# Performance work log

Measured on AMD Instinct MI355X. Metric: run time of the kernel, lower is better.

Reference implementation:

```python
import jax, jax.numpy as jnp
import numpy as np

N, E, B = 10000, 100000, 64
VOCAB, EMB, H = 5000, 100, 2000
LAYERS = 4


def setup_inputs() -> dict:
    key = jax.random.key(0)
    ks = jax.random.split(key, 12)
    s = 0.02
    tokens = jax.random.randint(ks[0], (N,), 0, VOCAB)
    edge_index = jax.random.randint(ks[1], (2, E), 0, N)
    batch = (jnp.arange(N) * B) // N  # sorted node->graph ids, every graph nonempty
    return {
        "tokens": tokens,
        "edge_index": edge_index,
        "batch": batch,
        "embed_table": jax.random.normal(ks[2], (VOCAB, EMB), jnp.float32) * s,
        "W_ggc": jax.random.normal(ks[3], (LAYERS, H, H), jnp.float32) * s,
        "W_ih": jax.random.normal(ks[4], (3 * H, H), jnp.float32) * s,
        "W_hh": jax.random.normal(ks[5], (3 * H, H), jnp.float32) * s,
        "b_ih": jnp.zeros((3 * H,), jnp.float32),
        "b_hh": jnp.zeros((3 * H,), jnp.float32),
        "conv1_w": jax.random.normal(ks[6], (50, 1, 3), jnp.float32) * s,
        "conv1_b": jnp.zeros((50,), jnp.float32),
        "conv2_w": jax.random.normal(ks[7], (100, 50, 3), jnp.float32) * s,
        "conv2_b": jnp.zeros((100,), jnp.float32),
        "conv3_w": jax.random.normal(ks[8], (150, 100, 3), jnp.float32) * s,
        "conv3_b": jnp.zeros((150,), jnp.float32),
        "lin1_w": jax.random.normal(ks[9], (500, 10950), jnp.float32) * s,
        "lin1_b": jnp.zeros((500,), jnp.float32),
        "lin2_w": jax.random.normal(ks[10], (4, 500), jnp.float32) * s,
        "lin2_b": jnp.zeros((4,), jnp.float32),
    }


def _conv1d(x, w, b):
    # x: [B, Cin, L], w: [Cout, Cin, K] -> [B, Cout, L-K+1] (VALID, like nn.Conv1d)
    y = jax.lax.conv_general_dilated(x, w, (1,), "VALID",
                                     dimension_numbers=("NCH", "OIH", "NCH"))
    return y + b[None, :, None]


def _maxpool3(x):
    # MaxPool1d(kernel=3, stride=3), floor mode (VALID)
    return jax.lax.reduce_window(x, -jnp.inf, jax.lax.max, (1, 1, 3), (1, 1, 3), "VALID")


def _gru_cell(m, h, W_ih, W_hh, b_ih, b_hh):
    gi = m @ W_ih.T + b_ih  # [N, 3H]
    gh = h @ W_hh.T + b_hh
    ir, iz, inn = jnp.split(gi, 3, axis=-1)
    hr, hz, hn = jnp.split(gh, 3, axis=-1)
    r = jax.nn.sigmoid(ir + hr)
    z = jax.nn.sigmoid(iz + hz)
    n = jnp.tanh(inn + r * hn)
    return (1.0 - z) * n + z * h


def reference(tokens, edge_index, batch, embed_table, W_ggc, W_ih, W_hh, b_ih, b_hh,
              conv1_w, conv1_b, conv2_w, conv2_b, conv3_w, conv3_b,
              lin1_w, lin1_b, lin2_w, lin2_b):
    src, dst = edge_index[0], edge_index[1]
    n_nodes = tokens.shape[0]
    # embedding + pad to GatedGraphConv width (PyG zero-pads when in < out)
    h = embed_table[tokens]                               # [N, 100]
    h = jnp.pad(h, ((0, 0), (0, H - h.shape[1])))         # [N, 2000]
    # GatedGraphConv: per-layer linear -> scatter-add over edges -> GRU update
    for i in range(LAYERS):
        m = h @ W_ggc[i]                                  # [N, H]
        agg = jax.ops.segment_sum(m[src], dst, num_segments=n_nodes)  # [N, H]
        h = _gru_cell(agg, h, W_ih, W_hh, b_ih, b_hh)
    x = jax.nn.relu(h)
    # global_max_pool over graphs
    pooled = jax.ops.segment_max(x, batch, num_segments=B)  # [B, 2000]
    x = pooled[:, None, :]                                  # [B, 1, 2000]
    x = _maxpool3(jax.nn.relu(_conv1d(x, conv1_w, conv1_b)))  # [B,50,666]
    x = _maxpool3(jax.nn.relu(_conv1d(x, conv2_w, conv2_b)))  # [B,100,221]
    x = _maxpool3(jax.nn.relu(_conv1d(x, conv3_w, conv3_b)))  # [B,150,73]
    x = x.reshape(x.shape[0], -1)                             # [B, 10950]
    x = jax.nn.relu(x @ lin1_w.T + lin1_b)
    # dropout is identity in eval mode
    x = jax.nn.relu(x @ lin2_w.T + lin2_b)
    return x
```

## Files before the change

### kernel.cpp

```cpp
#include <hip/hip_runtime.h>
#include <math.h>

#define N_NODES 10000
#define N_EDGES 100000
#define NB      64
#define EMB     100
#define H       2000
#define LAYERS  4

#define C1_OC 50
#define C1_L  666
#define C2_OC 100
#define C2_L  221
#define C3_OC 150
#define C3_L  73
#define LIN1_IN  10950
#define LIN1_OUT 500

#define SEG  2048
#define MP   10240
#define NW   2048
#define KK2  4096
#define NPACK 8192
#define NT   (KK2 / 64)

using half8 = __attribute__((ext_vector_type(8))) _Float16;
using f32x4 = __attribute__((ext_vector_type(4))) float;

__device__ inline void gload16(const void* g, void* l) {
  __builtin_amdgcn_global_load_lds(
      (const __attribute__((address_space(1))) unsigned int*)g,
      (__attribute__((address_space(3))) unsigned int*)l, 16, 0, 0);
}

__global__ void embed16_kernel(const int* __restrict__ tokens,
                               const float* __restrict__ table,
                               _Float16* __restrict__ h) {
  int n = blockIdx.x;
  int tok = tokens[n];
  for (int c = threadIdx.x; c < SEG; c += 256) {
    float v = (c < EMB) ? table[tok * EMB + c] : 0.f;
    h[(size_t)n * SEG + c] = (_Float16)v;
  }
}

__global__ void hist_kernel(const int* __restrict__ dst, int* __restrict__ counts, int e) {
  int i = blockIdx.x * 256 + threadIdx.x;
  if (i < e) atomicAdd(&counts[dst[i]], 1);
}

__global__ void scan_kernel(const int* __restrict__ counts, int* __restrict__ row_off, int n) {
  __shared__ int sums[1024];
  int tid = threadIdx.x;
  const int CH = (n + 1023) / 1024;
  int start = tid * CH;
  int local = 0;
  for (int i = 0; i < CH; i++)
    if (start + i < n) local += counts[start + i];
  sums[tid] = local;
  __syncthreads();
  for (int off = 1; off < 1024; off <<= 1) {
    int v = (tid >= off) ? sums[tid - off] : 0;
    __syncthreads();
    sums[tid] += v;
    __syncthreads();
  }
  int run = (tid > 0) ? sums[tid - 1] : 0;
  for (int i = 0; i < CH; i++)
    if (start + i < n) { row_off[start + i] = run; run += counts[start + i]; }
  if (tid == 1023) row_off[n] = run;
}

__global__ void scatter_kernel(const int* __restrict__ src, const int* __restrict__ dst,
                               const int* __restrict__ row_off, int* __restrict__ cursor,
                               int* __restrict__ csr_src, int e) {
  int i = blockIdx.x * 256 + threadIdx.x;
  if (i < e) {
    int d = dst[i];
    int pos = atomicAdd(&cursor[d], 1);
    csr_src[row_off[d] + pos] = src[i];
  }
}

__global__ void starts_kernel(const int* __restrict__ batch, int* __restrict__ starts, int n) {
  int i = blockIdx.x * 256 + threadIdx.x;
  if (i >= n) return;
  int b = batch[i];
  int pb = (i == 0) ? -1 : batch[i - 1];
  if (b != pb)
    for (int x = pb + 1; x <= b; x++) starts[x] = i;
  if (i == n - 1)
    for (int x = b + 1; x <= NB; x++) starts[x] = n;
}

__global__ void prep_wg16_kernel(const float* __restrict__ Wg, _Float16* __restrict__ out) {
  __shared__ float t[32][33];
  int l = blockIdx.z;
  const float* W = Wg + (size_t)l * H * H;
  _Float16* o = out + (size_t)l * NW * SEG;
  int kt = blockIdx.x * 32, nt = blockIdx.y * 32;
  int tx = threadIdx.x & 31, ty = threadIdx.x >> 5;
#pragma unroll
  for (int i = 0; i < 4; i++) {
    int k = kt + ty + i * 8, n = nt + tx;
    t[tx][ty + i * 8] = (k < H && n < H) ? W[(size_t)k * H + n] : 0.f;
  }
  __syncthreads();
#pragma unroll
  for (int i = 0; i < 4; i++) {
    int nl = ty + i * 8, kl = tx;
    o[(size_t)(nt + nl) * SEG + (kt + kl)] = (_Float16)t[nl][kl];
  }
}

__global__ void prep_wpack_kernel(const float* __restrict__ Wih, const float* __restrict__ Whh,
                                  _Float16* __restrict__ out) {
  int n = blockIdx.y;
  int k = blockIdx.x * 256 + threadIdx.x;
  if (k >= KK2) return;
  int gate = ((n >> 7) & 1) * 2 + ((n >> 4) & 1);
  int hcol = (n >> 8) * 64 + ((n >> 5) & 3) * 16 + (n & 15);
  float v = 0.f;
  if (hcol < H) {
    if (gate < 2) {
      int row = gate * H + hcol;
      if (k < 2048) { if (k < H) v = Wih[(size_t)row * H + k]; }
      else { int k2 = k - 2048; if (k2 < H) v = Whh[(size_t)row * H + k2]; }
    } else if (gate == 2) {
      if (k < H) v = Wih[(size_t)(2 * H + hcol) * H + k];
    } else {
      int k2 = k - 2048;
      if (k2 >= 0 && k2 < H) v = Whh[(size_t)(2 * H + hcol) * H + k2];
    }
  }
  out[(size_t)n * KK2 + k] = (_Float16)v;
}

__global__ __launch_bounds__(256) void gemm16_kernel(
    const _Float16* __restrict__ A, const _Float16* __restrict__ Bt,
    _Float16* __restrict__ C) {
  __shared__ __align__(16) _Float16 As[128][32];
  __shared__ __align__(16) _Float16 Bs[128][32];
  const int tid = threadIdx.x;
  const int wave = tid >> 6, lane = tid & 63;
  const int bm = blockIdx.y * 128, bn = blockIdx.x * 128;
  const int wm = (wave & 1) * 64, wn = (wave >> 1) * 64;
  const int srow = lane >> 2, scol = (lane & 3) * 8;
  const int fr = lane & 15, quad = lane >> 4;

  f32x4 acc[4][4];
#pragma unroll
  for (int i = 0; i < 4; i++)
#pragma unroll
    for (int j = 0; j < 4; j++) {
      f32x4 z = {0.f, 0.f, 0.f, 0.f};
      acc[i][j] = z;
    }

  for (int k0 = 0; k0 < SEG; k0 += 32) {
    gload16(A + (size_t)(bm + wave * 32 + srow) * SEG + k0 + scol, &As[wave * 32][0]);
    gload16(A + (size_t)(bm + wave * 32 + 16 + srow) * SEG + k0 + scol, &As[wave * 32 + 16][0]);
    gload16(Bt + (size_t)(bn + wave * 32 + srow) * SEG + k0 + scol, &Bs[wave * 32][0]);
    gload16(Bt + (size_t)(bn + wave * 32 + 16 + srow) * SEG + k0 + scol, &Bs[wave * 32 + 16][0]);
    __syncthreads();
    half8 af[4], bf[4];
#pragma unroll
    for (int i = 0; i < 4; i++) {
      af[i] = *(const half8*)&As[wm + i * 16 + fr][quad * 8];
      bf[i] = *(const half8*)&Bs[wn + i * 16 + fr][quad * 8];
    }
#pragma unroll
    for (int i = 0; i < 4; i++)
#pragma unroll
      for (int j = 0; j < 4; j++)
        acc[i][j] = __builtin_amdgcn_mfma_f32_16x16x32_f16(af[i], bf[j], acc[i][j], 0, 0, 0);
    __syncthreads();
  }
#pragma unroll
  for (int i = 0; i < 4; i++)
#pragma unroll
    for (int j = 0; j < 4; j++) {
      int n = bn + wn + j * 16 + fr;
      if (n >= SEG) continue;
#pragma unroll
      for (int r = 0; r < 4; r++) {
        int m = bm + wm + i * 16 + quad * 4 + r;
        C[(size_t)m * SEG + n] = (_Float16)acc[i][j][r];
      }
    }
}

__global__ void agg16_kernel(const _Float16* __restrict__ m, const int* __restrict__ row_off,
                             const int* __restrict__ csr_src, _Float16* __restrict__ agg) {
  int node = blockIdx.x;
  int s = row_off[node], e = row_off[node + 1];
  int tid = threadIdx.x;
  bool act = tid < (SEG / 8);
  float a[8] = {0, 0, 0, 0, 0, 0, 0, 0};
  __shared__ int s_src[256];
  for (int base = s; base < e; base += 256) {
    int cnt = min(256, e - base);
    __syncthreads();
    if (tid < cnt) s_src[tid] = csr_src[base + tid];
    __syncthreads();
    for (int p = 0; p < cnt; p++) {
      if (act) {
        half8 v = *(const half8*)&m[(size_t)s_src[p] * SEG + tid * 8];
#pragma unroll
        for (int i = 0; i < 8; i++) a[i] += (float)v[i];
      }
    }
  }
  if (act) {
    half8 o;
#pragma unroll
    for (int i = 0; i < 8; i++) o[i] = (_Float16)a[i];
    *(half8*)&agg[(size_t)node * SEG + tid * 8] = o;
  }
}

__global__ __launch_bounds__(512, 2) void gru8p_kernel(
    const _Float16* __restrict__ Agg, const _Float16* __restrict__ Hc,
    const _Float16* __restrict__ Wp,
    const float* __restrict__ b_ih, const float* __restrict__ b_hh,
    _Float16* __restrict__ Hn) {
  __shared__ __align__(16) _Float16 As[2][256][64];
  __shared__ __align__(16) _Float16 Bs[2][256][64];
  const int tid = threadIdx.x;
  const int wave = tid >> 6, lane = tid & 63;
  const int WM = wave >> 2, WN = wave & 3;
  const int fr = lane & 15, quad = lane >> 4;
  const int bm = blockIdx.y * 256, bn = blockIdx.x * 256;

  const int sr = lane >> 3;
  const int scl = (lane & 7) ^ sr;

  auto stageA = [&](int buf, int hf, int t) {
    const _Float16* base = (t < 32) ? Agg : Hc;
    const int k0 = (t & 31) * 64;
    const int r0 = hf * 128 + wave * 8 + sr;
#pragma unroll
    for (int c2 = 0; c2 < 2; c2++) {
      gload16(base + (size_t)(bm + r0 + c2 * 64) * SEG + k0 + scl * 8,
              &As[buf][hf * 128 + c2 * 64 + wave * 8][0]);
    }
  };
  auto stageB = [&](int buf, int hf, int t) {
    const int k0 = t * 64;
    const int r0 = hf * 128 + wave * 8 + sr;
#pragma unroll
    for (int c2 = 0; c2 < 2; c2++) {
      gload16(Wp + (size_t)(bn + r0 + c2 * 64) * KK2 + k0 + scl * 8,
              &Bs[buf][hf * 128 + c2 * 64 + wave * 8][0]);
    }
  };

  const int x0 = ((quad ^ (fr & 7)) << 3);
  const int x1 = (((quad + 4) ^ (fr & 7)) << 3);

  auto ldsA = [&](int buf, int mh, half8 (&af)[2][4]) {
    const _Float16* base = &As[buf][mh * 128 + WM * 64][0];
#pragma unroll
    for (int i = 0; i < 4; i++) {
      const int rb = ((i << 4) + fr) << 6;
      af[0][i] = *(const half8*)&base[rb + x0];
      af[1][i] = *(const half8*)&base[rb + x1];
    }
  };
  auto ldsB = [&](int buf, int nh, int j, half8 (&bf)[2]) {
    const _Float16* base = &Bs[buf][nh * 128 + WN * 32 + (j << 4) + fr][0];
    bf[0] = *(const half8*)&base[x0];
    bf[1] = *(const half8*)&base[x1];
  };

  f32x4 acc[2][4][4];
#pragma unroll
  for (int a = 0; a < 2; a++)
#pragma unroll
    for (int i = 0; i < 4; i++)
#pragma unroll
      for (int g = 0; g < 4; g++) {
        f32x4 z = {0.f, 0.f, 0.f, 0.f};
        acc[a][i][g] = z;
      }

  stageA(0, 0, 0); stageA(0, 1, 0); stageB(0, 0, 0); stageB(0, 1, 0);
  stageA(1, 0, 1); stageB(1, 0, 1);
  asm volatile("s_waitcnt vmcnt(4)" ::: "memory");
  __builtin_amdgcn_s_barrier();

  for (int t = 0; t < NT; t++) {
    const int cur = t & 1, nxt = cur ^ 1;
    const bool firstHalf = (t < 32);
#pragma unroll
    for (int mh = 0; mh < 2; mh++) {
      half8 af[2][4], b0[2], b1[2], bx[2];
      ldsA(cur, mh, af);
      ldsB(cur, 0, 0, b0);
      ldsB(cur, 0, 1, b1);
      if (mh == 0) { if (t + 1 < NT) stageA(nxt, 1, t + 1); }
      else         { if (t + 2 < NT) stageA(cur, 0, t + 2); }
      __builtin_amdgcn_s_barrier();
      asm volatile("s_waitcnt lgkmcnt(0)" ::: "memory");
      __builtin_amdgcn_sched_barrier(0);
      __builtin_amdgcn_s_setprio(1);
#pragma unroll
      for (int ks = 0; ks < 2; ks++)
#pragma unroll
        for (int i = 0; i < 4; i++) {
          acc[mh][i][0] = __builtin_amdgcn_mfma_f32_16x16x32_f16(af[ks][i], b0[ks], acc[mh][i][0], 0, 0, 0);
          acc[mh][i][1] = __builtin_amdgcn_mfma_f32_16x16x32_f16(af[ks][i], b1[ks], acc[mh][i][1], 0, 0, 0);
        }
      __builtin_amdgcn_s_setprio(0);
      __builtin_amdgcn_s_barrier();
      ldsB(cur, 1, firstHalf ? 0 : 1, bx);
      if (mh == 0) { if (t + 1 < NT) stageB(nxt, 1, t + 1); }
      else         { if (t + 2 < NT) stageB(cur, 0, t + 2); }
      __builtin_amdgcn_s_barrier();
      asm volatile("s_waitcnt lgkmcnt(0)" ::: "memory");
      __builtin_amdgcn_sched_barrier(0);
      __builtin_amdgcn_s_setprio(1);
      if (firstHalf) {
#pragma unroll
        for (int ks = 0; ks < 2; ks++)
#pragma unroll
          for (int i = 0; i < 4; i++)
            acc[mh][i][2] = __builtin_amdgcn_mfma_f32_16x16x32_f16(af[ks][i], bx[ks], acc[mh][i][2], 0, 0, 0);
      } else {
#pragma unroll
        for (int ks = 0; ks < 2; ks++)
#pragma unroll
          for (int i = 0; i < 4; i++)
            acc[mh][i][3] = __builtin_amdgcn_mfma_f32_16x16x32_f16(af[ks][i], bx[ks], acc[mh][i][3], 0, 0, 0);
      }
      __builtin_amdgcn_s_setprio(0);
      __builtin_amdgcn_s_barrier();
    }
    if (t + 2 < NT) {
      asm volatile("s_waitcnt vmcnt(4)" ::: "memory");
    } else if (t + 1 < NT) {
      asm volatile("s_waitcnt vmcnt(0)" ::: "memory");
    }
    __builtin_amdgcn_s_barrier();
  }

  const int c = blockIdx.x * 64 + WN * 16 + fr;
  if (c >= H) return;
  const float b_r = b_ih[c] + b_hh[c];
  const float b_z = b_ih[H + c] + b_hh[H + c];
  const float b_in = b_ih[2 * H + c];
  const float b_hn = b_hh[2 * H + c];
#pragma unroll
  for (int mh = 0; mh < 2; mh++)
#pragma unroll
    for (int i = 0; i < 4; i++)
#pragma unroll
      for (int r = 0; r < 4; r++) {
        int m = bm + mh * 128 + WM * 64 + i * 16 + quad * 4 + r;
        float rg = 1.f / (1.f + expf(-(acc[mh][i][0][r] + b_r)));
        float zg = 1.f / (1.f + expf(-(acc[mh][i][1][r] + b_z)));
        float nn = tanhf(acc[mh][i][2][r] + b_in + rg * (acc[mh][i][3][r] + b_hn));
        float hold = (float)Hc[(size_t)m * SEG + c];
        Hn[(size_t)m * SEG + c] = (_Float16)((1.f - zg) * nn + zg * hold);
      }
}

__global__ void pool16_kernel(const _Float16* __restrict__ h, const int* __restrict__ starts,
                              float* __restrict__ pooled) {
  int b = blockIdx.x;
  int s = starts[b], e = starts[b + 1];
  for (int idx = threadIdx.x; idx < H; idx += 256) {
    float mx = 0.f;
    for (int n = s; n < e; n++) mx = fmaxf(mx, (float)h[(size_t)n * SEG + idx]);
    pooled[b * H + idx] = mx;
  }
}

__global__ void conv1_kernel(const float* __restrict__ in, const float* __restrict__ w,
                             const float* __restrict__ bias, float* __restrict__ outp) {
  __shared__ float sin_[H];
  int b = blockIdx.x;
  for (int j = threadIdx.x; j < H; j += 256) sin_[j] = in[(size_t)b * H + j];
  __syncthreads();
  for (int idx = threadIdx.x; idx < C1_OC * C1_L; idx += 256) {
    int oc = idx / C1_L, t = idx % C1_L;
    float w0 = w[oc * 3], w1 = w[oc * 3 + 1], w2 = w[oc * 3 + 2];
    float bb = bias[oc];
    float best = 0.f;
    int base = t * 3;
#pragma unroll
    for (int p = 0; p < 3; p++) {
      float v = fmaf(sin_[base + p], w0, fmaf(sin_[base + p + 1], w1,
                fmaf(sin_[base + p + 2], w2, bb)));
      best = fmaxf(best, v);
    }
    outp[((size_t)b * C1_OC + oc) * C1_L + t] = best;
  }
}

__global__ void conv2_kernel(const float* __restrict__ in, const float* __restrict__ w,
                             const float* __restrict__ bias, float* __restrict__ outp) {
  int idx = blockIdx.x * 256 + threadIdx.x;
  if (idx >= NB * C2_OC * C2_L) return;
  int t = idx % C2_L;
  int rem = idx / C2_L;
  int oc = rem % C2_OC;
  int b = rem / C2_OC;
  const float* ip = in + (size_t)b * C1_OC * C1_L;
  const float* wp = w + oc * C1_OC * 3;
  float bb = bias[oc];
  float s0 = bb, s1 = bb, s2 = bb;
  int tc = t * 3;
  for (int ic = 0; ic < C1_OC; ic++) {
    const float* r = ip + ic * C1_L + tc;
    float v0 = r[0], v1 = r[1], v2 = r[2], v3 = r[3], v4 = r[4];
    float w0 = wp[ic * 3], w1 = wp[ic * 3 + 1], w2 = wp[ic * 3 + 2];
    s0 = fmaf(v0, w0, fmaf(v1, w1, fmaf(v2, w2, s0)));
    s1 = fmaf(v1, w0, fmaf(v2, w1, fmaf(v3, w2, s1)));
    s2 = fmaf(v2, w0, fmaf(v3, w1, fmaf(v4, w2, s2)));
  }
  outp[idx] = fmaxf(fmaxf(s0, fmaxf(s1, s2)), 0.f);
}

__global__ void conv3_kernel(const float* __restrict__ in, const float* __restrict__ w,
                             const float* __restrict__ bias, float* __restrict__ outp) {
  int idx = blockIdx.x * 256 + threadIdx.x;
  if (idx >= NB * C3_OC * C3_L) return;
  int t = idx % C3_L;
  int rem = idx / C3_L;
  int oc = rem % C3_OC;
  int b = rem / C3_OC;
  const float* ip = in + (size_t)b * C2_OC * C2_L;
  const float* wp = w + oc * C2_OC * 3;
  float bb = bias[oc];
  float s0 = bb, s1 = bb, s2 = bb;
  int tc = t * 3;
  for (int ic = 0; ic < C2_OC; ic++) {
    const float* r = ip + ic * C2_L + tc;
    float v0 = r[0], v1 = r[1], v2 = r[2], v3 = r[3], v4 = r[4];
    float w0 = wp[ic * 3], w1 = wp[ic * 3 + 1], w2 = wp[ic * 3 + 2];
    s0 = fmaf(v0, w0, fmaf(v1, w1, fmaf(v2, w2, s0)));
    s1 = fmaf(v1, w0, fmaf(v2, w1, fmaf(v3, w2, s1)));
    s2 = fmaf(v2, w0, fmaf(v3, w1, fmaf(v4, w2, s2)));
  }
  outp[idx] = fmaxf(fmaxf(s0, fmaxf(s1, s2)), 0.f);
}

__global__ void lin1_kernel(const float* __restrict__ x, const float* __restrict__ w,
                            const float* __restrict__ bias, float* __restrict__ outp) {
  int gid = blockIdx.x * 4 + (threadIdx.x >> 6);
  int lane = threadIdx.x & 63;
  int b = gid / LIN1_OUT;
  int o = gid % LIN1_OUT;
  const float* xp = x + (size_t)b * LIN1_IN;
  const float* wp = w + (size_t)o * LIN1_IN;
  float s = 0.f;
  for (int k = lane; k < LIN1_IN; k += 64) s = fmaf(xp[k], wp[k], s);
#pragma unroll
  for (int off = 32; off > 0; off >>= 1) s += __shfl_down(s, off, 64);
  if (lane == 0) outp[b * LIN1_OUT + o] = fmaxf(s + bias[o], 0.f);
}

__global__ void lin2_kernel(const float* __restrict__ x, const float* __restrict__ w,
                            const float* __restrict__ bias, float* __restrict__ outp) {
  int tid = threadIdx.x;
  int b = tid >> 2, o = tid & 3;
  const float* xp = x + b * LIN1_OUT;
  const float* wp = w + o * LIN1_OUT;
  float s = bias[o];
  for (int k = 0; k < LIN1_OUT; k++) s = fmaf(xp[k], wp[k], s);
  outp[b * 4 + o] = fmaxf(s, 0.f);
}

extern "C" void kernel_launch(void* const* d_in, const int* in_sizes, int n_in,
                              void* d_out, int out_size, void* d_ws, size_t ws_size,
                              hipStream_t stream) {
  const int* tokens = (const int*)d_in[0];
  const int* edge_index = (const int*)d_in[1];
  const int* batch = (const int*)d_in[2];
  const float* embed = (const float*)d_in[3];
  const float* W_ggc = (const float*)d_in[4];
  const float* W_ih = (const float*)d_in[5];
  const float* W_hh = (const float*)d_in[6];
  const float* b_ih = (const float*)d_in[7];
  const float* b_hh = (const float*)d_in[8];
  const float* c1w = (const float*)d_in[9];
  const float* c1b = (const float*)d_in[10];
  const float* c2w = (const float*)d_in[11];
  const float* c2b = (const float*)d_in[12];
  const float* c3w = (const float*)d_in[13];
  const float* c3b = (const float*)d_in[14];
  const float* l1w = (const float*)d_in[15];
  const float* l1b = (const float*)d_in[16];
  const float* l2w = (const float*)d_in[17];
  const float* l2b = (const float*)d_in[18];
  float* out = (float*)d_out;

  const int* e_src = edge_index;
  const int* e_dst = edge_index + N_EDGES;

  char* ws = (char*)d_ws;
  size_t off = 0;
  auto alloc = [&](size_t bytes) -> void* {
    void* p = ws + off;
    off = (off + bytes + 255) & ~(size_t)255;
    return p;
  };

  const size_t ACT = sizeof(_Float16) * (size_t)MP * SEG;
  _Float16* bufX = (_Float16*)alloc(ACT);
  _Float16* bufY = (_Float16*)alloc(ACT);
  _Float16* bufZ = (_Float16*)alloc(ACT);
  _Float16* Wg_b = (_Float16*)alloc(sizeof(_Float16) * (size_t)LAYERS * NW * SEG);
  _Float16* Wp   = (_Float16*)alloc(sizeof(_Float16) * (size_t)NPACK * KK2);
  int* counts = (int*)alloc(sizeof(int) * (N_NODES + 1));
  int* row_off = (int*)alloc(sizeof(int) * (N_NODES + 1));
  int* cursor = (int*)alloc(sizeof(int) * N_NODES);
  int* csr_src = (int*)alloc(sizeof(int) * N_EDGES);
  int* starts = (int*)alloc(sizeof(int) * (NB + 1));

  char* tb = (char*)bufZ;
  size_t toff = 0;
  auto talloc = [&](size_t bytes) -> void* {
    void* p = tb + toff;
    toff = (toff + bytes + 255) & ~(size_t)255;
    return p;
  };
  float* pooled = (float*)talloc(sizeof(float) * NB * H);
  float* c1 = (float*)talloc(sizeof(float) * (size_t)NB * C1_OC * C1_L);
  float* c2 = (float*)talloc(sizeof(float) * (size_t)NB * C2_OC * C2_L);
  float* c3 = (float*)talloc(sizeof(float) * (size_t)NB * C3_OC * C3_L);
  float* l1out = (float*)talloc(sizeof(float) * NB * LIN1_OUT);

  hipMemsetAsync(counts, 0, sizeof(int) * (N_NODES + 1), stream);
  hipMemsetAsync(cursor, 0, sizeof(int) * N_NODES, stream);

  {
    dim3 gg(SEG / 32, NW / 32, LAYERS);
    prep_wg16_kernel<<<gg, 256, 0, stream>>>(W_ggc, Wg_b);
    dim3 gp(KK2 / 256, NPACK);
    prep_wpack_kernel<<<gp, 256, 0, stream>>>(W_ih, W_hh, Wp);
  }

  embed16_kernel<<<N_NODES, 256, 0, stream>>>(tokens, embed, bufX);
  hist_kernel<<<(N_EDGES + 255) / 256, 256, 0, stream>>>(e_dst, counts, N_EDGES);
  scan_kernel<<<1, 1024, 0, stream>>>(counts, row_off, N_NODES);
  scatter_kernel<<<(N_EDGES + 255) / 256, 256, 0, stream>>>(e_src, e_dst, row_off, cursor,
                                                            csr_src, N_EDGES);
  starts_kernel<<<(N_NODES + 255) / 256, 256, 0, stream>>>(batch, starts, N_NODES);

  dim3 grid_m(NW / 128, MP / 128);
  dim3 grid_gru(NPACK / 256, MP / 256);
  _Float16* X = bufX;
  _Float16* Y = bufY;
  for (int l = 0; l < LAYERS; l++) {
    gemm16_kernel<<<grid_m, 256, 0, stream>>>(X, Wg_b + (size_t)l * NW * SEG, Y);
    agg16_kernel<<<N_NODES, 256, 0, stream>>>(Y, row_off, csr_src, bufZ);
    gru8p_kernel<<<grid_gru, 512, 0, stream>>>(bufZ, X, Wp, b_ih, b_hh, Y);
    _Float16* t = X; X = Y; Y = t;
  }

  pool16_kernel<<<NB, 256, 0, stream>>>(X, starts, pooled);
  conv1_kernel<<<NB, 256, 0, stream>>>(pooled, c1w, c1b, c1);
  conv2_kernel<<<(NB * C2_OC * C2_L + 255) / 256, 256, 0, stream>>>(c1, c2w, c2b, c2);
  conv3_kernel<<<(NB * C3_OC * C3_L + 255) / 256, 256, 0, stream>>>(c2, c3w, c3b, c3);
  lin1_kernel<<<NB * LIN1_OUT / 4, 256, 0, stream>>>(c3, l1w, l1b, l1out);
  lin2_kernel<<<1, 256, 0, stream>>>(l1out, l2w, l2b, out);
}
```

Baseline: 4.006 ms.

## Restructure GRU GEMM main loop into two-phase schedule with register prefetch of LDS fragments

Reorganizes the fused GRU GEMM inner loop from eight barrier-separated phases per K-tile to roughly two. LDS fragments for the next tile are read into registers while the current tile's MFMAs run, and the global-to-LDS stages for both halves are issued together. The aim is to cut barrier count and hide LDS read latency behind matrix work. In exchange it holds more fragments in registers, which raises register pressure at two waves per SIMD, and the buffer reuse ordering is more delicate.

New measurement: 4.744 ms. 1.18x slower.

```diff
diff --git a/kernel.cpp b/kernel.cpp
--- a/kernel.cpp
+++ b/kernel.cpp
@@ -219,7 +219,7 @@
   }
 }
 
-__global__ __launch_bounds__(512, 2) void gru8p_kernel(
+__global__ __launch_bounds__(512, 2) void gru2p_kernel(
     const _Float16* __restrict__ Agg, const _Float16* __restrict__ Hc,
     const _Float16* __restrict__ Wp,
     const float* __restrict__ b_ih, const float* __restrict__ b_hh,
@@ -258,19 +258,19 @@
   const int x0 = ((quad ^ (fr & 7)) << 3);
   const int x1 = (((quad + 4) ^ (fr & 7)) << 3);
 
-  auto ldsA = [&](int buf, int mh, half8 (&af)[2][4]) {
+  auto readA = [&](int buf, int mh, half8* a) {
     const _Float16* base = &As[buf][mh * 128 + WM * 64][0];
 #pragma unroll
     for (int i = 0; i < 4; i++) {
       const int rb = ((i << 4) + fr) << 6;
-      af[0][i] = *(const half8*)&base[rb + x0];
-      af[1][i] = *(const half8*)&base[rb + x1];
+      a[i]     = *(const half8*)&base[rb + x0];
+      a[4 + i] = *(const half8*)&base[rb + x1];
     }
   };
-  auto ldsB = [&](int buf, int nh, int j, half8 (&bf)[2]) {
+  auto readB = [&](int buf, int nh, int j, half8* b) {
     const _Float16* base = &Bs[buf][nh * 128 + WN * 32 + (j << 4) + fr][0];
-    bf[0] = *(const half8*)&base[x0];
-    bf[1] = *(const half8*)&base[x1];
+    b[0] = *(const half8*)&base[x0];
+    b[1] = *(const half8*)&base[x1];
   };
 
   f32x4 acc[2][4][4];
@@ -289,59 +289,87 @@
   asm volatile("s_waitcnt vmcnt(4)" ::: "memory");
   __builtin_amdgcn_s_barrier();
 
+  half8 a0[8], a1[8], b0[2], b1[2], bx[2], bxn[2];
+  readA(0, 0, a0);
+  readB(0, 0, 0, b0);
+  readB(0, 0, 1, b1);
+  readB(0, 1, 0, bx);
+
   for (int t = 0; t < NT; t++) {
     const int cur = t & 1, nxt = cur ^ 1;
     const bool firstHalf = (t < 32);
-#pragma unroll
-    for (int mh = 0; mh < 2; mh++) {
-      half8 af[2][4], b0[2], b1[2], bx[2];
-      ldsA(cur, mh, af);
-      ldsB(cur, 0, 0, b0);
-      ldsB(cur, 0, 1, b1);
-      if (mh == 0) { if (t + 1 < NT) stageA(nxt, 1, t + 1); }
-      else         { if (t + 2 < NT) stageA(cur, 0, t + 2); }
-      __builtin_amdgcn_s_barrier();
-      asm volatile("s_waitcnt lgkmcnt(0)" ::: "memory");
-      __builtin_amdgcn_sched_barrier(0);
-      __builtin_amdgcn_s_setprio(1);
-#pragma unroll
-      for (int ks = 0; ks < 2; ks++)
-#pragma unroll
-        for (int i = 0; i < 4; i++) {
-          acc[mh][i][0] = __builtin_amdgcn_mfma_f32_16x16x32_f16(af[ks][i], b0[ks], acc[mh][i][0], 0, 0, 0);
-          acc[mh][i][1] = __builtin_amdgcn_mfma_f32_16x16x32_f16(af[ks][i], b1[ks], acc[mh][i][1], 0, 0, 0);
-        }
-      __builtin_amdgcn_s_setprio(0);
-      __builtin_amdgcn_s_barrier();
-      ldsB(cur, 1, firstHalf ? 0 : 1, bx);
-      if (mh == 0) { if (t + 1 < NT) stageB(nxt, 1, t + 1); }
-      else         { if (t + 2 < NT) stageB(cur, 0, t + 2); }
-      __builtin_amdgcn_s_barrier();
-      asm volatile("s_waitcnt lgkmcnt(0)" ::: "memory");
-      __builtin_amdgcn_sched_barrier(0);
-      __builtin_amdgcn_s_setprio(1);
-      if (firstHalf) {
-#pragma unroll
-        for (int ks = 0; ks < 2; ks++)
-#pragma unroll
-          for (int i = 0; i < 4; i++)
-            acc[mh][i][2] = __builtin_amdgcn_mfma_f32_16x16x32_f16(af[ks][i], bx[ks], acc[mh][i][2], 0, 0, 0);
-      } else {
-#pragma unroll
-        for (int ks = 0; ks < 2; ks++)
-#pragma unroll
-          for (int i = 0; i < 4; i++)
-            acc[mh][i][3] = __builtin_amdgcn_mfma_f32_16x16x32_f16(af[ks][i], bx[ks], acc[mh][i][3], 0, 0, 0);
-      }
-      __builtin_amdgcn_s_setprio(0);
-      __builtin_amdgcn_s_barrier();
-    }
+
+    if (t + 1 < NT) { stageA(nxt, 1, t + 1); stageB(nxt, 1, t + 1); }
+    asm volatile("s_waitcnt lgkmcnt(0)" ::: "memory");
+    __builtin_amdgcn_sched_barrier(0);
+    __builtin_amdgcn_s_barrier();
+    readA(cur, 1, a1);
+    __builtin_amdgcn_sched_barrier(0);
+    __builtin_amdgcn_s_setprio(1);
+#pragma unroll
+    for (int i = 0; i < 4; i++) {
+      acc[0][i][0] = __builtin_amdgcn_mfma_f32_16x16x32_f16(a0[i], b0[0], acc[0][i][0], 0, 0, 0);
+      acc[0][i][1] = __builtin_amdgcn_mfma_f32_16x16x32_f16(a0[i], b1[0], acc[0][i][1], 0, 0, 0);
+      acc[0][i][0] = __builtin_amdgcn_mfma_f32_16x16x32_f16(a0[4 + i], b0[1], acc[0][i][0], 0, 0, 0);
+      acc[0][i][1] = __builtin_amdgcn_mfma_f32_16x16x32_f16(a0[4 + i], b1[1], acc[0][i][1], 0, 0, 0);
+    }
+    if (firstHalf) {
+#pragma unroll
+      for (int i = 0; i < 4; i++) {
+        acc[0][i][2] = __builtin_amdgcn_mfma_f32_16x16x32_f16(a0[i], bx[0], acc[0][i][2], 0, 0, 0);
+        acc[0][i][2] = __builtin_amdgcn_mfma_f32_16x16x32_f16(a0[4 + i], bx[1], acc[0][i][2], 0, 0, 0);
+      }
+    } else {
+#pragma unroll
+      for (int i = 0; i < 4; i++) {
+        acc[0][i][3] = __builtin_amdgcn_mfma_f32_16x16x32_f16(a0[i], bx[0], acc[0][i][3], 0, 0, 0);
+        acc[0][i][3] = __builtin_amdgcn_mfma_f32_16x16x32_f16(a0[4 + i], bx[1], acc[0][i][3], 0, 0, 0);
+      }
+    }
+    __builtin_amdgcn_s_setprio(0);
+
     if (t + 2 < NT) {
+      stageA(cur, 0, t + 2); stageB(cur, 0, t + 2);
       asm volatile("s_waitcnt vmcnt(4)" ::: "memory");
-    } else if (t + 1 < NT) {
+    } else {
       asm volatile("s_waitcnt vmcnt(0)" ::: "memory");
     }
+    asm volatile("s_waitcnt lgkmcnt(0)" ::: "memory");
+    __builtin_amdgcn_sched_barrier(0);
     __builtin_amdgcn_s_barrier();
+    __builtin_amdgcn_s_setprio(1);
+#pragma unroll
+    for (int i = 0; i < 4; i++) {
+      acc[1][i][0] = __builtin_amdgcn_mfma_f32_16x16x32_f16(a1[i], b0[0], acc[1][i][0], 0, 0, 0);
+      acc[1][i][1] = __builtin_amdgcn_mfma_f32_16x16x32_f16(a1[i], b1[0], acc[1][i][1], 0, 0, 0);
+      acc[1][i][0] = __builtin_amdgcn_mfma_f32_16x16x32_f16(a1[4 + i], b0[1], acc[1][i][0], 0, 0, 0);
+      acc[1][i][1] = __builtin_amdgcn_mfma_f32_16x16x32_f16(a1[4 + i], b1[1], acc[1][i][1], 0, 0, 0);
+    }
+    __builtin_amdgcn_s_setprio(0);
+    __builtin_amdgcn_sched_barrier(0);
+    if (t + 1 < NT) {
+      readA(nxt, 0, a0);
+      readB(nxt, 0, 0, b0);
+      readB(nxt, 0, 1, b1);
+      readB(nxt, 1, ((t + 1) < 32) ? 0 : 1, bxn);
+    }
+    __builtin_amdgcn_sched_barrier(0);
+    __builtin_amdgcn_s_setprio(1);
+    if (firstHalf) {
+#pragma unroll
+      for (int i = 0; i < 4; i++) {
+        acc[1][i][2] = __builtin_amdgcn_mfma_f32_16x16x32_f16(a1[i], bx[0], acc[1][i][2], 0, 0, 0);
+        acc[1][i][2] = __builtin_amdgcn_mfma_f32_16x16x32_f16(a1[4 + i], bx[1], acc[1][i][2], 0, 0, 0);
+      }
+    } else {
+#pragma unroll
+      for (int i = 0; i < 4; i++) {
+        acc[1][i][3] = __builtin_amdgcn_mfma_f32_16x16x32_f16(a1[i], bx[0], acc[1][i][3], 0, 0, 0);
+        acc[1][i][3] = __builtin_amdgcn_mfma_f32_16x16x32_f16(a1[4 + i], bx[1], acc[1][i][3], 0, 0, 0);
+      }
+    }
+    __builtin_amdgcn_s_setprio(0);
+    bx[0] = bxn[0]; bx[1] = bxn[1];
   }
 
   const int c = blockIdx.x * 64 + WN * 16 + fr;
@@ -556,7 +584,7 @@
   for (int l = 0; l < LAYERS; l++) {
     gemm16_kernel<<<grid_m, 256, 0, stream>>>(X, Wg_b + (size_t)l * NW * SEG, Y);
     agg16_kernel<<<N_NODES, 256, 0, stream>>>(Y, row_off, csr_src, bufZ);
-    gru8p_kernel<<<grid_gru, 512, 0, stream>>>(bufZ, X, Wp, b_ih, b_hh, Y);
+    gru2p_kernel<<<grid_gru, 512, 0, stream>>>(bufZ, X, Wp, b_ih, b_hh, Y);
     _Float16* t = X; X = Y; Y = t;
   }
 
```
